# Performance work log

Measured on AMD Instinct MI355X. Metric: run time of the kernel, lower is better.

The kernel has to match this reference:

```python
import jax, jax.numpy as jnp
import numpy as np

NUM_CHANNELS = 32  # matches fill_max of ch_ids


def setup_inputs() -> dict:
    key = jax.random.key(0)
    k1, k2 = jax.random.split(key)
    z = jax.random.normal(k1, (4096, 1, 64, 128), dtype=jnp.float32)
    ch_ids = jax.random.randint(k2, (4096,), 0, NUM_CHANNELS, dtype=jnp.int64)
    return {"z": z, "ch_ids": ch_ids}


def reference(z, ch_ids):
    # z: (B, 1, N, D) -> squeeze -> (B, N, D)
    z = jnp.squeeze(z, axis=1)
    B = z.shape[0]
    # Per-channel mean via segment sum (reduction='mean')
    sums = jax.ops.segment_sum(z, ch_ids, num_segments=NUM_CHANNELS)        # (C, N, D)
    counts = jax.ops.segment_sum(jnp.ones((B,), z.dtype), ch_ids,
                                 num_segments=NUM_CHANNELS)                  # (C,)
    mean = sums / jnp.maximum(counts, 1.0)[:, None, None]                    # (C, N, D)
    # Broadcast mean back to each row of its channel, concat on patch dim
    aggr = mean[ch_ids]                                                      # (B, N, D)
    return jnp.concatenate([z, aggr], axis=-2)                               # (B, 2N, D)
```

## Files before the change

### kernel.cpp

```cpp
#include <hip/hip_runtime.h>

#define NB      4096
#define NCH     32
#define ND      8192
#define OUTROW  16384
#define NSPLIT  8
#define NCHUNK  8

__global__ void build_lists_kernel(const int* __restrict__ ch,
                                   int* __restrict__ counts,
                                   int* __restrict__ lists) {
    int b = blockIdx.x * blockDim.x + threadIdx.x;
    if (b < NB) {
        int c = ch[b];
        int pos = atomicAdd(&counts[c], 1);
        lists[c * NB + pos] = b;
    }
}

__global__ __launch_bounds__(256) void copy_reduce_kernel(
        const float* __restrict__ z,
        const int* __restrict__ counts,
        const int* __restrict__ lists,
        float* __restrict__ out,
        float* __restrict__ sums) {
    const int bid   = blockIdx.x;
    const int s     = bid & (NSPLIT - 1);
    const int chunk = (bid / NSPLIT) & (NCHUNK - 1);
    const int c     = bid / (NSPLIT * NCHUNK);
    const int off   = chunk * 1024 + threadIdx.x * 4;
    const int cnt   = counts[c];
    const int* __restrict__ lst = lists + c * NB;

    float4 acc = make_float4(0.f, 0.f, 0.f, 0.f);

    int i = s;
    for (; i + 3 * NSPLIT < cnt; i += 4 * NSPLIT) {
        const int b0 = lst[i];
        const int b1 = lst[i +     NSPLIT];
        const int b2 = lst[i + 2 * NSPLIT];
        const int b3 = lst[i + 3 * NSPLIT];
        const float4 v0 = *(const float4*)(z + (long)b0 * ND + off);
        const float4 v1 = *(const float4*)(z + (long)b1 * ND + off);
        const float4 v2 = *(const float4*)(z + (long)b2 * ND + off);
        const float4 v3 = *(const float4*)(z + (long)b3 * ND + off);
        *(float4*)(out + (long)b0 * OUTROW + off) = v0;
        *(float4*)(out + (long)b1 * OUTROW + off) = v1;
        *(float4*)(out + (long)b2 * OUTROW + off) = v2;
        *(float4*)(out + (long)b3 * OUTROW + off) = v3;
        acc.x += (v0.x + v1.x) + (v2.x + v3.x);
        acc.y += (v0.y + v1.y) + (v2.y + v3.y);
        acc.z += (v0.z + v1.z) + (v2.z + v3.z);
        acc.w += (v0.w + v1.w) + (v2.w + v3.w);
    }
    for (; i < cnt; i += NSPLIT) {
        const int b = lst[i];
        const float4 v = *(const float4*)(z + (long)b * ND + off);
        *(float4*)(out + (long)b * OUTROW + off) = v;
        acc.x += v.x; acc.y += v.y; acc.z += v.z; acc.w += v.w;
    }

    float* dst = sums + (long)c * ND + off;
    atomicAdd(dst + 0, acc.x);
    atomicAdd(dst + 1, acc.y);
    atomicAdd(dst + 2, acc.z);
    atomicAdd(dst + 3, acc.w);
}

__global__ __launch_bounds__(256) void broadcast_kernel(
        const int* __restrict__ counts,
        const int* __restrict__ lists,
        const float* __restrict__ sums,
        float* __restrict__ out) {
    const int bid   = blockIdx.x;
    const int s     = bid & (NSPLIT - 1);
    const int chunk = (bid / NSPLIT) & (NCHUNK - 1);
    const int c     = bid / (NSPLIT * NCHUNK);
    const int off   = chunk * 1024 + threadIdx.x * 4;
    const int cnt   = counts[c];
    const int* __restrict__ lst = lists + c * NB;

    const float inv = 1.0f / fmaxf((float)cnt, 1.0f);
    float4 m = *(const float4*)(sums + (long)c * ND + off);
    m.x *= inv; m.y *= inv; m.z *= inv; m.w *= inv;

    int i = s;
    for (; i + 3 * NSPLIT < cnt; i += 4 * NSPLIT) {
        const int b0 = lst[i];
        const int b1 = lst[i +     NSPLIT];
        const int b2 = lst[i + 2 * NSPLIT];
        const int b3 = lst[i + 3 * NSPLIT];
        *(float4*)(out + (long)b0 * OUTROW + ND + off) = m;
        *(float4*)(out + (long)b1 * OUTROW + ND + off) = m;
        *(float4*)(out + (long)b2 * OUTROW + ND + off) = m;
        *(float4*)(out + (long)b3 * OUTROW + ND + off) = m;
    }
    for (; i < cnt; i += NSPLIT) {
        const int b = lst[i];
        *(float4*)(out + (long)b * OUTROW + ND + off) = m;
    }
}

extern "C" void kernel_launch(void* const* d_in, const int* in_sizes, int n_in,
                              void* d_out, int out_size, void* d_ws, size_t ws_size,
                              hipStream_t stream) {
    const float* z  = (const float*)d_in[0];
    const int*   ch = (const int*)d_in[1];
    float*       out = (float*)d_out;

    int*   counts = (int*)d_ws;
    float* sums   = (float*)((char*)d_ws + 128);
    int*   lists  = (int*)((char*)d_ws + 128 + (size_t)NCH * ND * sizeof(float));

    hipMemsetAsync(d_ws, 0, 128 + (size_t)NCH * ND * sizeof(float), stream);
    build_lists_kernel<<<(NB + 255) / 256, 256, 0, stream>>>(ch, counts, lists);

    const int grid = NCH * NCHUNK * NSPLIT;
    copy_reduce_kernel<<<grid, 256, 0, stream>>>(z, counts, lists, out, sums);
    broadcast_kernel<<<grid, 256, 0, stream>>>(counts, lists, sums, out);
}
```

Baseline: 386.2 us.

## Fuse copy-reduce and broadcast kernels with last-block completion counter

Merges the copy/reduce and broadcast kernels into one launch. Each block atomically bumps a per-(channel,chunk) counter after adding its partial sums, and the last of the NSPLIT blocks computes the mean and writes it to every row of that channel. This removes one kernel launch and the grid-wide barrier between the phases. In exchange, the broadcast for each chunk is done by a single block instead of eight, which serializes those writes and may reduce parallelism in the output-heavy half.

Result: slower. 876.5 us (+126.9%).

```diff
diff --git a/kernel.cpp b/kernel.cpp
--- a/kernel.cpp
+++ b/kernel.cpp
@@ -18,12 +18,13 @@
     }
 }
 
-__global__ __launch_bounds__(256) void copy_reduce_kernel(
+__global__ __launch_bounds__(256) void mixer_kernel(
         const float* __restrict__ z,
         const int* __restrict__ counts,
         const int* __restrict__ lists,
-        float* __restrict__ out,
-        float* __restrict__ sums) {
+        float* __restrict__ sums,
+        int* __restrict__ done,
+        float* __restrict__ out) {
     const int bid   = blockIdx.x;
     const int s     = bid & (NSPLIT - 1);
     const int chunk = (bid / NSPLIT) & (NCHUNK - 1);
@@ -65,38 +66,36 @@
     atomicAdd(dst + 1, acc.y);
     atomicAdd(dst + 2, acc.z);
     atomicAdd(dst + 3, acc.w);
-}
 
-__global__ __launch_bounds__(256) void broadcast_kernel(
-        const int* __restrict__ counts,
-        const int* __restrict__ lists,
-        const float* __restrict__ sums,
-        float* __restrict__ out) {
-    const int bid   = blockIdx.x;
-    const int s     = bid & (NSPLIT - 1);
-    const int chunk = (bid / NSPLIT) & (NCHUNK - 1);
-    const int c     = bid / (NSPLIT * NCHUNK);
-    const int off   = chunk * 1024 + threadIdx.x * 4;
-    const int cnt   = counts[c];
-    const int* __restrict__ lst = lists + c * NB;
+    __threadfence();
+    __syncthreads();
 
+    __shared__ int last;
+    if (threadIdx.x == 0) {
+        int old = atomicAdd(&done[c * NCHUNK + chunk], 1);
+        last = (old == NSPLIT - 1) ? 1 : 0;
+    }
+    __syncthreads();
+    if (!last) return;
+
+    __threadfence();
     const float inv = 1.0f / fmaxf((float)cnt, 1.0f);
     float4 m = *(const float4*)(sums + (long)c * ND + off);
     m.x *= inv; m.y *= inv; m.z *= inv; m.w *= inv;
 
-    int i = s;
-    for (; i + 3 * NSPLIT < cnt; i += 4 * NSPLIT) {
-        const int b0 = lst[i];
-        const int b1 = lst[i +     NSPLIT];
-        const int b2 = lst[i + 2 * NSPLIT];
-        const int b3 = lst[i + 3 * NSPLIT];
+    int j = 0;
+    for (; j + 4 <= cnt; j += 4) {
+        const int b0 = lst[j + 0];
+        const int b1 = lst[j + 1];
+        const int b2 = lst[j + 2];
+        const int b3 = lst[j + 3];
         *(float4*)(out + (long)b0 * OUTROW + ND + off) = m;
         *(float4*)(out + (long)b1 * OUTROW + ND + off) = m;
         *(float4*)(out + (long)b2 * OUTROW + ND + off) = m;
         *(float4*)(out + (long)b3 * OUTROW + ND + off) = m;
     }
-    for (; i < cnt; i += NSPLIT) {
-        const int b = lst[i];
+    for (; j < cnt; ++j) {
+        const int b = lst[j];
         *(float4*)(out + (long)b * OUTROW + ND + off) = m;
     }
 }
@@ -109,13 +108,12 @@
     float*       out = (float*)d_out;
 
     int*   counts = (int*)d_ws;
-    float* sums   = (float*)((char*)d_ws + 128);
-    int*   lists  = (int*)((char*)d_ws + 128 + (size_t)NCH * ND * sizeof(float));
+    int*   done   = (int*)((char*)d_ws + 128);
+    float* sums   = (float*)((char*)d_ws + 8192);
+    int*   lists  = (int*)((char*)d_ws + 8192 + (size_t)NCH * ND * sizeof(float));
 
-    hipMemsetAsync(d_ws, 0, 128 + (size_t)NCH * ND * sizeof(float), stream);
+    hipMemsetAsync(d_ws, 0, 8192 + (size_t)NCH * ND * sizeof(float), stream);
     build_lists_kernel<<<(NB + 255) / 256, 256, 0, stream>>>(ch, counts, lists);
-
-    const int grid = NCH * NCHUNK * NSPLIT;
-    copy_reduce_kernel<<<grid, 256, 0, stream>>>(z, counts, lists, out, sums);
-    broadcast_kernel<<<grid, 256, 0, stream>>>(counts, lists, sums, out);
+    mixer_kernel<<<NCH * NCHUNK * NSPLIT, 256, 0, stream>>>(z, counts, lists,
+                                                            sums, done, out);
 }
```

## Split reduce into partial-sum scratch, finalize means, then streaming row-ordered write

Applied to the files above, without the earlier changes.

The reduction kernel no longer copies z into the output. It writes per-split partial sums into unused output rows, which serve as scratch, so the float atomics and the large memset of the sums buffer go away. A finalize kernel adds up the partials and scales them into a compact means buffer. A new write kernel then walks rows in batch order, copying z and the gathered means with nontemporal stores. z is now read twice (reduce and write), but the output writes become sequential and streaming instead of scattered, at the cost of one extra kernel launch.

After: 387.7 us. About the same (+0.4%).

```diff
diff --git a/kernel.cpp b/kernel.cpp
--- a/kernel.cpp
+++ b/kernel.cpp
@@ -6,6 +6,9 @@
 #define OUTROW  16384
 #define NSPLIT  8
 #define NCHUNK  8
+#define ROWS_B  16
+
+typedef __attribute__((ext_vector_type(4))) float f4;
 
 __global__ void build_lists_kernel(const int* __restrict__ ch,
                                    int* __restrict__ counts,
@@ -18,21 +21,20 @@
     }
 }
 
-__global__ __launch_bounds__(256) void copy_reduce_kernel(
+__global__ __launch_bounds__(256) void reduce_kernel(
         const float* __restrict__ z,
         const int* __restrict__ counts,
         const int* __restrict__ lists,
-        float* __restrict__ out,
-        float* __restrict__ sums) {
+        float* __restrict__ out) {
     const int bid   = blockIdx.x;
     const int s     = bid & (NSPLIT - 1);
-    const int chunk = (bid / NSPLIT) & (NCHUNK - 1);
-    const int c     = bid / (NSPLIT * NCHUNK);
+    const int chunk = (bid >> 3) & (NCHUNK - 1);
+    const int c     = bid >> 6;
     const int off   = chunk * 1024 + threadIdx.x * 4;
     const int cnt   = counts[c];
     const int* __restrict__ lst = lists + c * NB;
 
-    float4 acc = make_float4(0.f, 0.f, 0.f, 0.f);
+    f4 acc = (f4)(0.0f);
 
     int i = s;
     for (; i + 3 * NSPLIT < cnt; i += 4 * NSPLIT) {
@@ -40,64 +42,71 @@
         const int b1 = lst[i +     NSPLIT];
         const int b2 = lst[i + 2 * NSPLIT];
         const int b3 = lst[i + 3 * NSPLIT];
-        const float4 v0 = *(const float4*)(z + (long)b0 * ND + off);
-        const float4 v1 = *(const float4*)(z + (long)b1 * ND + off);
-        const float4 v2 = *(const float4*)(z + (long)b2 * ND + off);
-        const float4 v3 = *(const float4*)(z + (long)b3 * ND + off);
-        *(float4*)(out + (long)b0 * OUTROW + off) = v0;
-        *(float4*)(out + (long)b1 * OUTROW + off) = v1;
-        *(float4*)(out + (long)b2 * OUTROW + off) = v2;
-        *(float4*)(out + (long)b3 * OUTROW + off) = v3;
-        acc.x += (v0.x + v1.x) + (v2.x + v3.x);
-        acc.y += (v0.y + v1.y) + (v2.y + v3.y);
-        acc.z += (v0.z + v1.z) + (v2.z + v3.z);
-        acc.w += (v0.w + v1.w) + (v2.w + v3.w);
+        const f4 v0 = *(const f4*)(z + (long)b0 * ND + off);
+        const f4 v1 = *(const f4*)(z + (long)b1 * ND + off);
+        const f4 v2 = *(const f4*)(z + (long)b2 * ND + off);
+        const f4 v3 = *(const f4*)(z + (long)b3 * ND + off);
+        acc += (v0 + v1) + (v2 + v3);
     }
     for (; i < cnt; i += NSPLIT) {
         const int b = lst[i];
-        const float4 v = *(const float4*)(z + (long)b * ND + off);
-        *(float4*)(out + (long)b * OUTROW + off) = v;
-        acc.x += v.x; acc.y += v.y; acc.z += v.z; acc.w += v.w;
+        acc += *(const f4*)(z + (long)b * ND + off);
     }
 
-    float* dst = sums + (long)c * ND + off;
-    atomicAdd(dst + 0, acc.x);
-    atomicAdd(dst + 1, acc.y);
-    atomicAdd(dst + 2, acc.z);
-    atomicAdd(dst + 3, acc.w);
+    *(f4*)(out + (long)(c * NSPLIT + s) * OUTROW + ND + off) = acc;
 }
 
-__global__ __launch_bounds__(256) void broadcast_kernel(
+__global__ __launch_bounds__(256) void finalize_kernel(
         const int* __restrict__ counts,
-        const int* __restrict__ lists,
-        const float* __restrict__ sums,
+        const float* __restrict__ out,
+        float* __restrict__ means) {
+    const long idx = ((long)blockIdx.x * 256 + threadIdx.x) * 4;
+    const int  c   = (int)(idx >> 13);
+    const int  d   = (int)(idx & (ND - 1));
+    const float* __restrict__ p = out + (long)(c * NSPLIT) * OUTROW + ND + d;
+
+    f4 a = (f4)(0.0f);
+#pragma unroll
+    for (int s = 0; s < NSPLIT; ++s)
+        a += *(const f4*)(p + (long)s * OUTROW);
+
+    const float inv = 1.0f / fmaxf((float)counts[c], 1.0f);
+    a *= inv;
+    *(f4*)(means + idx) = a;
+}
+
+__global__ __launch_bounds__(256) void write_kernel(
+        const float* __restrict__ z,
+        const int* __restrict__ ch,
+        const float* __restrict__ means,
         float* __restrict__ out) {
     const int bid   = blockIdx.x;
-    const int s     = bid & (NSPLIT - 1);
-    const int chunk = (bid / NSPLIT) & (NCHUNK - 1);
-    const int c     = bid / (NSPLIT * NCHUNK);
+    const int chunk = bid & (NCHUNK - 1);
+    const int b0    = (bid >> 3) * ROWS_B;
     const int off   = chunk * 1024 + threadIdx.x * 4;
-    const int cnt   = counts[c];
-    const int* __restrict__ lst = lists + c * NB;
 
-    const float inv = 1.0f / fmaxf((float)cnt, 1.0f);
-    float4 m = *(const float4*)(sums + (long)c * ND + off);
-    m.x *= inv; m.y *= inv; m.z *= inv; m.w *= inv;
+    int cv[ROWS_B];
+#pragma unroll
+    for (int r = 0; r < ROWS_B; ++r) cv[r] = ch[b0 + r];
 
-    int i = s;
-    for (; i + 3 * NSPLIT < cnt; i += 4 * NSPLIT) {
-        const int b0 = lst[i];
-        const int b1 = lst[i +     NSPLIT];
-        const int b2 = lst[i + 2 * NSPLIT];
-        const int b3 = lst[i + 3 * NSPLIT];
-        *(float4*)(out + (long)b0 * OUTROW + ND + off) = m;
-        *(float4*)(out + (long)b1 * OUTROW + ND + off) = m;
-        *(float4*)(out + (long)b2 * OUTROW + ND + off) = m;
-        *(float4*)(out + (long)b3 * OUTROW + ND + off) = m;
-    }
-    for (; i < cnt; i += NSPLIT) {
-        const int b = lst[i];
-        *(float4*)(out + (long)b * OUTROW + ND + off) = m;
+#pragma unroll
+    for (int r = 0; r < ROWS_B; r += 4) {
+        const f4 v0 = *(const f4*)(z + (long)(b0 + r + 0) * ND + off);
+        const f4 v1 = *(const f4*)(z + (long)(b0 + r + 1) * ND + off);
+        const f4 v2 = *(const f4*)(z + (long)(b0 + r + 2) * ND + off);
+        const f4 v3 = *(const f4*)(z + (long)(b0 + r + 3) * ND + off);
+        const f4 m0 = *(const f4*)(means + (long)cv[r + 0] * ND + off);
+        const f4 m1 = *(const f4*)(means + (long)cv[r + 1] * ND + off);
+        const f4 m2 = *(const f4*)(means + (long)cv[r + 2] * ND + off);
+        const f4 m3 = *(const f4*)(means + (long)cv[r + 3] * ND + off);
+        __builtin_nontemporal_store(v0, (f4*)(out + (long)(b0 + r + 0) * OUTROW + off));
+        __builtin_nontemporal_store(v1, (f4*)(out + (long)(b0 + r + 1) * OUTROW + off));
+        __builtin_nontemporal_store(v2, (f4*)(out + (long)(b0 + r + 2) * OUTROW + off));
+        __builtin_nontemporal_store(v3, (f4*)(out + (long)(b0 + r + 3) * OUTROW + off));
+        __builtin_nontemporal_store(m0, (f4*)(out + (long)(b0 + r + 0) * OUTROW + ND + off));
+        __builtin_nontemporal_store(m1, (f4*)(out + (long)(b0 + r + 1) * OUTROW + ND + off));
+        __builtin_nontemporal_store(m2, (f4*)(out + (long)(b0 + r + 2) * OUTROW + ND + off));
+        __builtin_nontemporal_store(m3, (f4*)(out + (long)(b0 + r + 3) * OUTROW + ND + off));
     }
 }
 
@@ -109,13 +118,12 @@
     float*       out = (float*)d_out;
 
     int*   counts = (int*)d_ws;
-    float* sums   = (float*)((char*)d_ws + 128);
-    int*   lists  = (int*)((char*)d_ws + 128 + (size_t)NCH * ND * sizeof(float));
+    float* means  = (float*)((char*)d_ws + 8192);
+    int*   lists  = (int*)((char*)d_ws + 8192 + (size_t)NCH * ND * sizeof(float));
 
-    hipMemsetAsync(d_ws, 0, 128 + (size_t)NCH * ND * sizeof(float), stream);
+    hipMemsetAsync(counts, 0, 128, stream);
     build_lists_kernel<<<(NB + 255) / 256, 256, 0, stream>>>(ch, counts, lists);
-
-    const int grid = NCH * NCHUNK * NSPLIT;
-    copy_reduce_kernel<<<grid, 256, 0, stream>>>(z, counts, lists, out, sums);
-    broadcast_kernel<<<grid, 256, 0, stream>>>(counts, lists, sums, out);
+    reduce_kernel<<<NCH * NCHUNK * NSPLIT, 256, 0, stream>>>(z, counts, lists, out);
+    finalize_kernel<<<NCH * ND / 1024, 256, 0, stream>>>(counts, out, means);
+    write_kernel<<<(NB / ROWS_B) * NCHUNK, 256, 0, stream>>>(z, ch, means, out);
 }
```
